# Optimization experiments

Measured on AMD Instinct MI355X. Metric: run time of the kernel, lower is better.

Reference implementation:

```python
import jax, jax.numpy as jnp
import numpy as np

EPS = 1e-08
SIGMA = 0.1
B = 1.0


def setup_inputs() -> dict:
    key = jax.random.key(0)
    k1, k2 = jax.random.split(key)
    N, C, H, W = 4, 256, 64, 64
    featureT = jax.random.normal(k1, (N, C, H, W), dtype=jnp.float32)
    featureI = jax.random.normal(k2, (N, C, H, W), dtype=jnp.float32)
    return {"featureT": featureT, "featureI": featureI}


def reference(featureT, featureI):
    N, C, H, W = featureT.shape
    # center both by target mean over (batch, spatial)
    meanT = featureT.mean(axis=(0, 2, 3), keepdims=True)
    fI = featureI - meanT
    fT = featureT - meanT
    # channel-wise L2 normalize
    fI = fI / (jnp.linalg.norm(fI, axis=1, keepdims=True) + EPS)
    fT = fT / (jnp.linalg.norm(fT, axis=1, keepdims=True) + EPS)
    # 1x1-patch conv2d == contraction over channels: sim[n, p, h, w]
    # where p indexes the flattened H*W spatial positions of the target.
    fT_flat = fT.reshape(N, C, H * W)  # [N, C, P]
    sim = jnp.einsum('nchw,ncp->nphw', fI, fT_flat)  # [N, P, H, W]
    raw_dist = (1.0 - sim) / 2.0
    # relative distances: divide by min over patch axis
    div = jnp.min(raw_dist, axis=1, keepdims=True)
    relative_dist = raw_dist / (div + EPS)
    # contextual similarity: exp-weight + sum-normalize over patch axis
    Wt = jnp.exp((B - relative_dist) / (SIGMA + EPS))
    W_sum = Wt.sum(axis=1, keepdims=True)
    CX = Wt / (W_sum + EPS)
    # max over spatial dims of featureI, mean over patches, -log, mean over batch
    CX = CX.max(axis=(2, 3))           # [N, P]
    CX = CX.mean(axis=1)               # [N]
    CX_loss = -jnp.log(CX + EPS)
    return jnp.mean(CX_loss)
```

## Files before the change

### kernel.cpp

```cpp
#include <hip/hip_runtime.h>
#include <cmath>


#define NB 4
#define CC 256
#define HW 4096
#define NQ0 8
#define NCS 16

static constexpr float kEPS = 1e-8f;
static constexpr float kSIG = 0.1f + 1e-8f;

typedef __attribute__((ext_vector_type(8)))  short short8;
typedef __attribute__((ext_vector_type(16))) float f32x16;

enum {
  OFF_MEAN = 0,
  OFF_CMAX = 256,
  OFF_WSUM = OFF_CMAX + NQ0*NB*HW,
  OFF_MAXP = OFF_WSUM + NQ0*NB*HW,
  OFF_MAXV = OFF_MAXP + NCS*NB*HW,
  OFF_GT   = OFF_MAXV + NB*HW,
  OFF_GI   = OFF_GT + NB*HW*CC/2,
  WS_FLOATS_FULL = OFF_GI + NB*HW*CC/2
};

__device__ __forceinline__ ushort cvt_bf16(float x) {
  unsigned u = __float_as_uint(x);
  unsigned r = (u + 0x7fffu + ((u >> 16) & 1u)) >> 16;
  return (ushort)r;
}

__device__ __forceinline__ void glds16(const ushort* g, ushort* l) {
  __builtin_amdgcn_global_load_lds(
      (const __attribute__((address_space(1))) unsigned*)g,
      (__attribute__((address_space(3))) unsigned*)l, 16, 0, 0);
}
__device__ __forceinline__ void s_bar()  { asm volatile("s_barrier" ::: "memory"); }
__device__ __forceinline__ void w_vm8()  { asm volatile("s_waitcnt vmcnt(8)" ::: "memory"); }
__device__ __forceinline__ void w_vm0()  { asm volatile("s_waitcnt vmcnt(0)" ::: "memory"); }
__device__ __forceinline__ void w_lgkm() { asm volatile("s_waitcnt lgkmcnt(0)" ::: "memory"); }

__device__ __forceinline__ float blockSum256(float v) {
  __shared__ float sh[4];
  const int lane = threadIdx.x & 63, wv = threadIdx.x >> 6;
  #pragma unroll
  for (int o = 32; o > 0; o >>= 1) v += __shfl_down(v, o, 64);
  __syncthreads();
  if (lane == 0) sh[wv] = v;
  __syncthreads();
  return sh[0] + sh[1] + sh[2] + sh[3];
}

__global__ __launch_bounds__(256) void k_mean9(const float* __restrict__ fT,
                                               float* __restrict__ ws) {
  const int c = blockIdx.x, t = threadIdx.x;
  float s = 0.f;
  for (int n = 0; n < NB; ++n) {
    const float* p = fT + (size_t)(n*CC + c)*HW;
    #pragma unroll
    for (int k = 0; k < 16; ++k) s += p[k*256 + t];
  }
  const float tot = blockSum256(s);
  if (t == 0) ws[OFF_MEAN + c] = tot * (1.0f/16384.0f);
}

__global__ __launch_bounds__(256) void k_prep9(const float* __restrict__ fT,
                                               const float* __restrict__ fI,
                                               float* __restrict__ ws) {
  __shared__ float stage[32][257];
  __shared__ float prt[8][32];
  __shared__ float sinv[32];
  const int t = threadIdx.x, l = t & 63;
  int bid = blockIdx.x;
  const int tensor = (bid >= 512); bid &= 511;
  const int n   = bid >> 7;
  const int r32 = bid & 127;
  const int p0  = r32 * 32;

  const float* __restrict__ src = tensor ? fI : fT;
  ushort* __restrict__ dst = (ushort*)(ws + (tensor ? OFF_GI : OFF_GT));
  const float* __restrict__ mean = ws + OFF_MEAN;

  const int pl = t & 31, cg = t >> 5;
  float acc = 0.f;
  #pragma unroll
  for (int i = 0; i < 32; ++i) {
    const int c = cg*32 + i;
    const float v = src[((size_t)(n*CC + c))*HW + p0 + pl] - mean[c];
    stage[pl][c] = v;
    acc += v*v;
  }
  prt[cg][pl] = acc;
  __syncthreads();
  if (t < 32) {
    float s = 0.f;
    #pragma unroll
    for (int g = 0; g < 8; ++g) s += prt[g][t];
    sinv[t] = 1.0f/(sqrtf(s) + kEPS);
  }
  __syncthreads();

  const int w = t >> 6, lhi = l >> 5, m = l & 31;
  const float iv = sinv[m];
  #pragma unroll
  for (int i = 0; i < 4; ++i) {
    const int kc = w*4 + i;
    const int cb = kc*16 + lhi*8;
    short8 o;
    #pragma unroll
    for (int j = 0; j < 8; ++j)
      ((ushort*)&o)[j] = cvt_bf16(stage[m][cb + j] * iv);
    *(short8*)(dst + (((size_t)(n*128 + r32)*16 + kc) << 9) + l*8) = o;
  }
}


#define SWEEP_IDS                                                             \
  const int t = threadIdx.x;                                                  \
  const int w = t >> 6, l = t & 63;                                           \
  const int ln31 = l & 31, lhi = l >> 5;  (void)lhi;                          \
  const int L = blockIdx.x;                                                   \
  const int xcd = L & 7, g = L >> 3;                                          \
  const int nh = xcd*4 + (g & 3);                                             \
  const int cs = g >> 2;                                                      \
  const int n = nh >> 3, h = nh & 7;                                          \
  const int col0 = cs * 256;

#define LOAD_BREG                                                             \
  short8 breg0[16], breg1[16];                                                \
  {                                                                           \
    const int RB0 = cs*8 + w, RB1 = cs*8 + 4 + w;                             \
    _Pragma("unroll")                                                         \
    for (int kc = 0; kc < 16; ++kc) {                                         \
      breg0[kc] = *(const short8*)(gB + (((size_t)(n*128 + RB0)*16 + kc) << 9) + l*8); \
      breg1[kc] = *(const short8*)(gB + (((size_t)(n*128 + RB1)*16 + kc) << 9) + l*8); \
    }                                                                         \
  }

#define STAGE_TILE(it_, buf_)                                                 \
  {                                                                           \
    const ushort* __restrict__ srcg = gAn + ((size_t)(it_) << 14);            \
    ushort* __restrict__ dstl = &Ab[buf_][0];                                 \
    _Pragma("unroll")                                                         \
    for (int i = 0; i < 8; ++i)                                               \
      glds16(srcg + (size_t)(i*256 + t)*8, dstl + (i*256 + t)*8);             \
  }

__global__ __launch_bounds__(256, 2) void k_gA(
    const ushort* __restrict__ gA, const ushort* __restrict__ gB,
    float* __restrict__ ws)
{
  __shared__ ushort Ab[2][16384];
  __shared__ float red2[256];

  SWEEP_IDS
  const ushort* __restrict__ gAn = gA + ((size_t)(n*128 + h*16) << 13);

  STAGE_TILE(0, 0)
  STAGE_TILE(1, 1)
  LOAD_BREG

  float run0 = -3.0e38f, run1 = -3.0e38f;

  for (int it = 0; it < 8; ++it) {
    if (it < 7) w_vm8(); else w_vm0();
    s_bar();

    const ushort* __restrict__ Abuf = &Ab[it & 1][0];
    f32x16 acc00, acc01, acc10, acc11;
    #pragma unroll
    for (int e = 0; e < 16; ++e) { acc00[e]=0.f; acc01[e]=0.f; acc10[e]=0.f; acc11[e]=0.f; }
    #pragma unroll
    for (int kc = 0; kc < 16; ++kc) {
      const short8 a0 = *(const short8*)&Abuf[kc*512 + l*8];
      const short8 a1 = *(const short8*)&Abuf[8192 + kc*512 + l*8];
      acc00 = __builtin_amdgcn_mfma_f32_32x32x16_bf16(a0, breg0[kc], acc00, 0, 0, 0);
      acc01 = __builtin_amdgcn_mfma_f32_32x32x16_bf16(a0, breg1[kc], acc01, 0, 0, 0);
      acc10 = __builtin_amdgcn_mfma_f32_32x32x16_bf16(a1, breg0[kc], acc10, 0, 0, 0);
      acc11 = __builtin_amdgcn_mfma_f32_32x32x16_bf16(a1, breg1[kc], acc11, 0, 0, 0);
    }
    w_lgkm();
    s_bar();
    if (it + 2 < 8) STAGE_TILE(it + 2, it & 1)

    #pragma unroll
    for (int r = 0; r < 16; ++r) {
      run0 = fmaxf(run0, fmaxf(acc00[r], acc10[r]));
      run1 = fmaxf(run1, fmaxf(acc01[r], acc11[r]));
    }
  }

  run0 = fmaxf(run0, __shfl_xor(run0, 32, 64));
  run1 = fmaxf(run1, __shfl_xor(run1, 32, 64));
  if (l < 32) {
    red2[w*32 + ln31]       = run0;
    red2[128 + w*32 + ln31] = run1;
  }
  __syncthreads();
  ws[OFF_CMAX + h*(NB*HW) + n*HW + col0 + t] = red2[t];
}

__global__ __launch_bounds__(256, 2) void k_gB(
    const ushort* __restrict__ gA, const ushort* __restrict__ gB,
    float* __restrict__ ws)
{
  __shared__ ushort Ab[2][16384];
  __shared__ float red2[256];

  SWEEP_IDS
  const ushort* __restrict__ gAn = gA + ((size_t)(n*128 + h*16) << 13);

  STAGE_TILE(0, 0)
  STAGE_TILE(1, 1)

  float aq0, bq0, aq1, bq1;
  {
    const int q0 = col0 + w*32 + ln31;
    const int q1 = q0 + 128;
    float cm0 = -3.0e38f, cm1 = -3.0e38f;
    #pragma unroll
    for (int hh = 0; hh < NQ0; ++hh) {
      cm0 = fmaxf(cm0, ws[OFF_CMAX + hh*(NB*HW) + n*HW + q0]);
      cm1 = fmaxf(cm1, ws[OFF_CMAX + hh*(NB*HW) + n*HW + q1]);
    }
    const float i0 = 1.0f/(2.0f*(0.5f*(1.0f - cm0) + kEPS));
    const float i1 = 1.0f/(2.0f*(0.5f*(1.0f - cm1) + kEPS));
    bq0 = i0 / kSIG; aq0 = (1.0f - i0) / kSIG;
    bq1 = i1 / kSIG; aq1 = (1.0f - i1) / kSIG;
  }

  LOAD_BREG

  float ws0 = 0.f, ws1 = 0.f;

  for (int it = 0; it < 8; ++it) {
    if (it < 7) w_vm8(); else w_vm0();
    s_bar();

    const ushort* __restrict__ Abuf = &Ab[it & 1][0];
    f32x16 acc00, acc01, acc10, acc11;
    #pragma unroll
    for (int e = 0; e < 16; ++e) { acc00[e]=0.f; acc01[e]=0.f; acc10[e]=0.f; acc11[e]=0.f; }
    #pragma unroll
    for (int kc = 0; kc < 16; ++kc) {
      const short8 a0 = *(const short8*)&Abuf[kc*512 + l*8];
      const short8 a1 = *(const short8*)&Abuf[8192 + kc*512 + l*8];
      acc00 = __builtin_amdgcn_mfma_f32_32x32x16_bf16(a0, breg0[kc], acc00, 0, 0, 0);
      acc01 = __builtin_amdgcn_mfma_f32_32x32x16_bf16(a0, breg1[kc], acc01, 0, 0, 0);
      acc10 = __builtin_amdgcn_mfma_f32_32x32x16_bf16(a1, breg0[kc], acc10, 0, 0, 0);
      acc11 = __builtin_amdgcn_mfma_f32_32x32x16_bf16(a1, breg1[kc], acc11, 0, 0, 0);
    }
    w_lgkm();
    s_bar();
    if (it + 2 < 8) STAGE_TILE(it + 2, it & 1)

    #pragma unroll
    for (int r = 0; r < 16; ++r) {
      ws0 += __expf(fmaf(bq0, acc00[r], aq0));
      ws0 += __expf(fmaf(bq0, acc10[r], aq0));
      ws1 += __expf(fmaf(bq1, acc01[r], aq1));
      ws1 += __expf(fmaf(bq1, acc11[r], aq1));
    }
  }

  ws0 += __shfl_xor(ws0, 32, 64);
  ws1 += __shfl_xor(ws1, 32, 64);
  if (l < 32) {
    red2[w*32 + ln31]       = ws0;
    red2[128 + w*32 + ln31] = ws1;
  }
  __syncthreads();
  ws[OFF_WSUM + h*(NB*HW) + n*HW + col0 + t] = red2[t];
}

__global__ __launch_bounds__(256, 2) void k_gC(
    const ushort* __restrict__ gA, const ushort* __restrict__ gB,
    float* __restrict__ ws)
{
  __shared__ ushort Ab[2][16384];
  __shared__ float gam_s[256], bet_s[256];
  __shared__ float stash[4][512];

  SWEEP_IDS
  const ushort* __restrict__ gAn = gA + ((size_t)(n*128 + h*16) << 13);

  STAGE_TILE(0, 0)
  STAGE_TILE(1, 1)

  {
    const int idx = n*HW + col0 + t;
    float cm = -3.0e38f;
    #pragma unroll
    for (int hh = 0; hh < NQ0; ++hh)
      cm = fmaxf(cm, ws[OFF_CMAX + hh*(NB*HW) + idx]);
    float sw = 0.f;
    #pragma unroll
    for (int hh = 0; hh < NQ0; ++hh)
      sw += ws[OFF_WSUM + hh*(NB*HW) + idx];
    const float i0 = 1.0f/(2.0f*(0.5f*(1.0f - cm) + kEPS));
    bet_s[t] = i0 / kSIG;
    gam_s[t] = (1.0f - i0) / kSIG - logf(sw + kEPS);
  }

  LOAD_BREG
  __syncthreads();

  for (int it = 0; it < 8; ++it) {
    if (it < 7) w_vm8(); else w_vm0();
    s_bar();

    const ushort* __restrict__ Abuf = &Ab[it & 1][0];
    f32x16 acc00, acc01, acc10, acc11;
    #pragma unroll
    for (int e = 0; e < 16; ++e) { acc00[e]=0.f; acc01[e]=0.f; acc10[e]=0.f; acc11[e]=0.f; }
    #pragma unroll
    for (int kc = 0; kc < 16; ++kc) {
      const short8 a0 = *(const short8*)&Abuf[kc*512 + l*8];
      const short8 a1 = *(const short8*)&Abuf[8192 + kc*512 + l*8];
      acc00 = __builtin_amdgcn_mfma_f32_32x32x16_bf16(breg0[kc], a0, acc00, 0, 0, 0);
      acc01 = __builtin_amdgcn_mfma_f32_32x32x16_bf16(breg0[kc], a1, acc01, 0, 0, 0);
      acc10 = __builtin_amdgcn_mfma_f32_32x32x16_bf16(breg1[kc], a0, acc10, 0, 0, 0);
      acc11 = __builtin_amdgcn_mfma_f32_32x32x16_bf16(breg1[kc], a1, acc11, 0, 0, 0);
    }
    w_lgkm();
    s_bar();
    if (it + 2 < 8) STAGE_TILE(it + 2, it & 1)

    float m0 = -3.0e38f, m1 = -3.0e38f;
    #pragma unroll
    for (int r = 0; r < 16; ++r) {
      const int row = (r & 3) + 8*(r >> 2) + 4*lhi;
      const float g0v = gam_s[w*32 + row],       b0v = bet_s[w*32 + row];
      const float g1v = gam_s[128 + w*32 + row], b1v = bet_s[128 + w*32 + row];
      m0 = fmaxf(m0, fmaf(b0v, acc00[r], g0v));
      m0 = fmaxf(m0, fmaf(b1v, acc10[r], g1v));
      m1 = fmaxf(m1, fmaf(b0v, acc01[r], g0v));
      m1 = fmaxf(m1, fmaf(b1v, acc11[r], g1v));
    }
    m0 = fmaxf(m0, __shfl_xor(m0, 32, 64));
    m1 = fmaxf(m1, __shfl_xor(m1, 32, 64));
    if (l < 32) {
      stash[w][it*64 + ln31]      = m0;
      stash[w][it*64 + 32 + ln31] = m1;
    }
  }

  __syncthreads();
  float* __restrict__ MAXP = ws + OFF_MAXP + (size_t)cs*(NB*HW) + n*HW + h*512;
  #pragma unroll
  for (int p = t; p < 512; p += 256) {
    MAXP[p] = fmaxf(fmaxf(stash[0][p], stash[1][p]),
                    fmaxf(stash[2][p], stash[3][p]));
  }
}

__global__ __launch_bounds__(256) void k_red(float* __restrict__ ws) {
  const int idx = blockIdx.x*256 + threadIdx.x;
  float m = ws[OFF_MAXP + idx];
  #pragma unroll
  for (int s = 1; s < NCS; ++s)
    m = fmaxf(m, ws[OFF_MAXP + s*(NB*HW) + idx]);
  ws[OFF_MAXV + idx] = m;
}

__global__ __launch_bounds__(256) void k_final9(const float* __restrict__ ws,
                                                float* __restrict__ out) {
  const int t = threadIdx.x;
  float loss = 0.f;
  for (int n = 0; n < NB; ++n) {
    float s = 0.f;
    for (int k = 0; k < 16; ++k)
      s += __expf(ws[OFF_MAXV + n*HW + k*256 + t]);
    const float tot = blockSum256(s);
    loss += -logf(tot*(1.0f/4096.0f) + kEPS);
  }
  if (t == 0) out[0] = loss*0.25f;
}

extern "C" void kernel_launch(void* const* d_in, const int* in_sizes, int n_in,
                              void* d_out, int out_size, void* d_ws, size_t ws_size,
                              hipStream_t stream) {
  const float* fT = (const float*)d_in[0];
  const float* fI = (const float*)d_in[1];
  float* out = (float*)d_out;
  float* ws  = (float*)d_ws;

  const size_t need_full = (size_t)WS_FLOATS_FULL * sizeof(float);
  if (ws_size < need_full) return;

  const ushort* GT = (const ushort*)(ws + OFF_GT);
  const ushort* GI = (const ushort*)(ws + OFF_GI);
  k_mean9 <<<256,  256, 0, stream>>>(fT, ws);
  k_prep9 <<<1024, 256, 0, stream>>>(fT, fI, ws);
  k_gA    <<<512,  256, 0, stream>>>(GT, GI, ws);
  k_gB    <<<512,  256, 0, stream>>>(GT, GI, ws);
  k_gC    <<<512,  256, 0, stream>>>(GT, GI, ws);
  k_red   <<<64,   256, 0, stream>>>(ws);
  k_final9<<<1,    256, 0, stream>>>(ws, out);
}
```

Before: 178.1 us.

## Switch GEMM sweeps to triple-buffered half-size A tiles with one barrier per step

The three sweep kernels now stage 32-row A tiles instead of 64-row ones, in a 3-deep LDS ring, over 16 iterations instead of 8. The next-next tile is issued right after the single barrier, which drops the second barrier and the lgkm wait per iteration. MFMA sections are wrapped in s_setprio to favour issue. The aim is better overlap of global-to-LDS loads with compute and less sync overhead. In exchange each MFMA block is shorter, so loop and epilogue overhead is paid twice as often.

Result: no change. 178.7 us (+0.3%).

```diff
diff --git a/kernel.cpp b/kernel.cpp
--- a/kernel.cpp
+++ b/kernel.cpp
@@ -37,9 +37,8 @@
       (__attribute__((address_space(3))) unsigned*)l, 16, 0, 0);
 }
 __device__ __forceinline__ void s_bar()  { asm volatile("s_barrier" ::: "memory"); }
-__device__ __forceinline__ void w_vm8()  { asm volatile("s_waitcnt vmcnt(8)" ::: "memory"); }
+__device__ __forceinline__ void w_vm4()  { asm volatile("s_waitcnt vmcnt(4)" ::: "memory"); }
 __device__ __forceinline__ void w_vm0()  { asm volatile("s_waitcnt vmcnt(0)" ::: "memory"); }
-__device__ __forceinline__ void w_lgkm() { asm volatile("s_waitcnt lgkmcnt(0)" ::: "memory"); }
 
 __device__ __forceinline__ float blockSum256(float v) {
   __shared__ float sh[4];
@@ -140,10 +139,10 @@
 
 #define STAGE_TILE(it_, buf_)                                                 \
   {                                                                           \
-    const ushort* __restrict__ srcg = gAn + ((size_t)(it_) << 14);            \
+    const ushort* __restrict__ srcg = gAn + ((size_t)(it_) << 13);            \
     ushort* __restrict__ dstl = &Ab[buf_][0];                                 \
     _Pragma("unroll")                                                         \
-    for (int i = 0; i < 8; ++i)                                               \
+    for (int i = 0; i < 4; ++i)                                               \
       glds16(srcg + (size_t)(i*256 + t)*8, dstl + (i*256 + t)*8);             \
   }
 
@@ -151,7 +150,7 @@
     const ushort* __restrict__ gA, const ushort* __restrict__ gB,
     float* __restrict__ ws)
 {
-  __shared__ ushort Ab[2][16384];
+  __shared__ ushort Ab[3][8192];
   __shared__ float red2[256];
 
   SWEEP_IDS
@@ -163,32 +162,33 @@
 
   float run0 = -3.0e38f, run1 = -3.0e38f;
 
-  for (int it = 0; it < 8; ++it) {
-    if (it < 7) w_vm8(); else w_vm0();
+  int cur = 0, nxt2 = 2;
+  for (int iter = 0; iter < 16; ++iter) {
+    if (iter < 15) w_vm4(); else w_vm0();
     s_bar();
 
-    const ushort* __restrict__ Abuf = &Ab[it & 1][0];
-    f32x16 acc00, acc01, acc10, acc11;
-    #pragma unroll
-    for (int e = 0; e < 16; ++e) { acc00[e]=0.f; acc01[e]=0.f; acc10[e]=0.f; acc11[e]=0.f; }
+    if (iter + 2 < 16) STAGE_TILE(iter + 2, nxt2)
+
+    const ushort* __restrict__ Abuf = &Ab[cur][0];
+    f32x16 acc0, acc1;
+    #pragma unroll
+    for (int e = 0; e < 16; ++e) { acc0[e] = 0.f; acc1[e] = 0.f; }
+    __builtin_amdgcn_s_setprio(1);
     #pragma unroll
     for (int kc = 0; kc < 16; ++kc) {
       const short8 a0 = *(const short8*)&Abuf[kc*512 + l*8];
-      const short8 a1 = *(const short8*)&Abuf[8192 + kc*512 + l*8];
-      acc00 = __builtin_amdgcn_mfma_f32_32x32x16_bf16(a0, breg0[kc], acc00, 0, 0, 0);
-      acc01 = __builtin_amdgcn_mfma_f32_32x32x16_bf16(a0, breg1[kc], acc01, 0, 0, 0);
-      acc10 = __builtin_amdgcn_mfma_f32_32x32x16_bf16(a1, breg0[kc], acc10, 0, 0, 0);
-      acc11 = __builtin_amdgcn_mfma_f32_32x32x16_bf16(a1, breg1[kc], acc11, 0, 0, 0);
-    }
-    w_lgkm();
-    s_bar();
-    if (it + 2 < 8) STAGE_TILE(it + 2, it & 1)
+      acc0 = __builtin_amdgcn_mfma_f32_32x32x16_bf16(a0, breg0[kc], acc0, 0, 0, 0);
+      acc1 = __builtin_amdgcn_mfma_f32_32x32x16_bf16(a0, breg1[kc], acc1, 0, 0, 0);
+    }
+    __builtin_amdgcn_s_setprio(0);
 
     #pragma unroll
     for (int r = 0; r < 16; ++r) {
-      run0 = fmaxf(run0, fmaxf(acc00[r], acc10[r]));
-      run1 = fmaxf(run1, fmaxf(acc01[r], acc11[r]));
-    }
+      run0 = fmaxf(run0, acc0[r]);
+      run1 = fmaxf(run1, acc1[r]);
+    }
+    cur  = (cur  == 2) ? 0 : cur + 1;
+    nxt2 = (nxt2 == 2) ? 0 : nxt2 + 1;
   }
 
   run0 = fmaxf(run0, __shfl_xor(run0, 32, 64));
@@ -205,7 +205,7 @@
     const ushort* __restrict__ gA, const ushort* __restrict__ gB,
     float* __restrict__ ws)
 {
-  __shared__ ushort Ab[2][16384];
+  __shared__ ushort Ab[3][8192];
   __shared__ float red2[256];
 
   SWEEP_IDS
@@ -234,34 +234,33 @@
 
   float ws0 = 0.f, ws1 = 0.f;
 
-  for (int it = 0; it < 8; ++it) {
-    if (it < 7) w_vm8(); else w_vm0();
+  int cur = 0, nxt2 = 2;
+  for (int iter = 0; iter < 16; ++iter) {
+    if (iter < 15) w_vm4(); else w_vm0();
     s_bar();
 
-    const ushort* __restrict__ Abuf = &Ab[it & 1][0];
-    f32x16 acc00, acc01, acc10, acc11;
-    #pragma unroll
-    for (int e = 0; e < 16; ++e) { acc00[e]=0.f; acc01[e]=0.f; acc10[e]=0.f; acc11[e]=0.f; }
+    if (iter + 2 < 16) STAGE_TILE(iter + 2, nxt2)
+
+    const ushort* __restrict__ Abuf = &Ab[cur][0];
+    f32x16 acc0, acc1;
+    #pragma unroll
+    for (int e = 0; e < 16; ++e) { acc0[e] = 0.f; acc1[e] = 0.f; }
+    __builtin_amdgcn_s_setprio(1);
     #pragma unroll
     for (int kc = 0; kc < 16; ++kc) {
       const short8 a0 = *(const short8*)&Abuf[kc*512 + l*8];
-      const short8 a1 = *(const short8*)&Abuf[8192 + kc*512 + l*8];
-      acc00 = __builtin_amdgcn_mfma_f32_32x32x16_bf16(a0, breg0[kc], acc00, 0, 0, 0);
-      acc01 = __builtin_amdgcn_mfma_f32_32x32x16_bf16(a0, breg1[kc], acc01, 0, 0, 0);
-      acc10 = __builtin_amdgcn_mfma_f32_32x32x16_bf16(a1, breg0[kc], acc10, 0, 0, 0);
-      acc11 = __builtin_amdgcn_mfma_f32_32x32x16_bf16(a1, breg1[kc], acc11, 0, 0, 0);
-    }
-    w_lgkm();
-    s_bar();
-    if (it + 2 < 8) STAGE_TILE(it + 2, it & 1)
+      acc0 = __builtin_amdgcn_mfma_f32_32x32x16_bf16(a0, breg0[kc], acc0, 0, 0, 0);
+      acc1 = __builtin_amdgcn_mfma_f32_32x32x16_bf16(a0, breg1[kc], acc1, 0, 0, 0);
+    }
+    __builtin_amdgcn_s_setprio(0);
 
     #pragma unroll
     for (int r = 0; r < 16; ++r) {
-      ws0 += __expf(fmaf(bq0, acc00[r], aq0));
-      ws0 += __expf(fmaf(bq0, acc10[r], aq0));
-      ws1 += __expf(fmaf(bq1, acc01[r], aq1));
-      ws1 += __expf(fmaf(bq1, acc11[r], aq1));
-    }
+      ws0 += __expf(fmaf(bq0, acc0[r], aq0));
+      ws1 += __expf(fmaf(bq1, acc1[r], aq1));
+    }
+    cur  = (cur  == 2) ? 0 : cur + 1;
+    nxt2 = (nxt2 == 2) ? 0 : nxt2 + 1;
   }
 
   ws0 += __shfl_xor(ws0, 32, 64);
@@ -278,7 +277,7 @@
     const ushort* __restrict__ gA, const ushort* __restrict__ gB,
     float* __restrict__ ws)
 {
-  __shared__ ushort Ab[2][16384];
+  __shared__ ushort Ab[3][8192];
   __shared__ float gam_s[256], bet_s[256];
   __shared__ float stash[4][512];
 
@@ -306,44 +305,40 @@
   LOAD_BREG
   __syncthreads();
 
-  for (int it = 0; it < 8; ++it) {
-    if (it < 7) w_vm8(); else w_vm0();
+  int cur = 0, nxt2 = 2;
+  for (int iter = 0; iter < 16; ++iter) {
+    if (iter < 15) w_vm4(); else w_vm0();
     s_bar();
 
-    const ushort* __restrict__ Abuf = &Ab[it & 1][0];
-    f32x16 acc00, acc01, acc10, acc11;
-    #pragma unroll
-    for (int e = 0; e < 16; ++e) { acc00[e]=0.f; acc01[e]=0.f; acc10[e]=0.f; acc11[e]=0.f; }
+    if (iter + 2 < 16) STAGE_TILE(iter + 2, nxt2)
+
+    const ushort* __restrict__ Abuf = &Ab[cur][0];
+    f32x16 accq0, accq1;
+    #pragma unroll
+    for (int e = 0; e < 16; ++e) { accq0[e] = 0.f; accq1[e] = 0.f; }
+    __builtin_amdgcn_s_setprio(1);
     #pragma unroll
     for (int kc = 0; kc < 16; ++kc) {
       const short8 a0 = *(const short8*)&Abuf[kc*512 + l*8];
-      const short8 a1 = *(const short8*)&Abuf[8192 + kc*512 + l*8];
-      acc00 = __builtin_amdgcn_mfma_f32_32x32x16_bf16(breg0[kc], a0, acc00, 0, 0, 0);
-      acc01 = __builtin_amdgcn_mfma_f32_32x32x16_bf16(breg0[kc], a1, acc01, 0, 0, 0);
-      acc10 = __builtin_amdgcn_mfma_f32_32x32x16_bf16(breg1[kc], a0, acc10, 0, 0, 0);
-      acc11 = __builtin_amdgcn_mfma_f32_32x32x16_bf16(breg1[kc], a1, acc11, 0, 0, 0);
-    }
-    w_lgkm();
-    s_bar();
-    if (it + 2 < 8) STAGE_TILE(it + 2, it & 1)
-
-    float m0 = -3.0e38f, m1 = -3.0e38f;
+      accq0 = __builtin_amdgcn_mfma_f32_32x32x16_bf16(breg0[kc], a0, accq0, 0, 0, 0);
+      accq1 = __builtin_amdgcn_mfma_f32_32x32x16_bf16(breg1[kc], a0, accq1, 0, 0, 0);
+    }
+    __builtin_amdgcn_s_setprio(0);
+
+    float m = -3.0e38f;
     #pragma unroll
     for (int r = 0; r < 16; ++r) {
       const int row = (r & 3) + 8*(r >> 2) + 4*lhi;
       const float g0v = gam_s[w*32 + row],       b0v = bet_s[w*32 + row];
       const float g1v = gam_s[128 + w*32 + row], b1v = bet_s[128 + w*32 + row];
-      m0 = fmaxf(m0, fmaf(b0v, acc00[r], g0v));
-      m0 = fmaxf(m0, fmaf(b1v, acc10[r], g1v));
-      m1 = fmaxf(m1, fmaf(b0v, acc01[r], g0v));
-      m1 = fmaxf(m1, fmaf(b1v, acc11[r], g1v));
-    }
-    m0 = fmaxf(m0, __shfl_xor(m0, 32, 64));
-    m1 = fmaxf(m1, __shfl_xor(m1, 32, 64));
-    if (l < 32) {
-      stash[w][it*64 + ln31]      = m0;
-      stash[w][it*64 + 32 + ln31] = m1;
-    }
+      m = fmaxf(m, fmaf(b0v, accq0[r], g0v));
+      m = fmaxf(m, fmaf(b1v, accq1[r], g1v));
+    }
+    m = fmaxf(m, __shfl_xor(m, 32, 64));
+    if (l < 32) stash[w][iter*32 + ln31] = m;
+
+    cur  = (cur  == 2) ? 0 : cur + 1;
+    nxt2 = (nxt2 == 2) ? 0 : nxt2 + 1;
   }
 
   __syncthreads();
```
